# Performance work log

Measured on AMD Instinct MI355X. Metric: run time of the kernel, lower is better.

The kernel has to match this reference:

```python
import jax, jax.numpy as jnp
import numpy as np

BATCH, SEQ, STATE, OBS, INP = 4096, 512, 16, 8, 4


def setup_inputs() -> dict:
    key = jax.random.key(0)
    ks = jax.random.split(key, 5)
    # scale A to spectral radius ~0.3 so the 512-step recursion is stable
    A = jax.random.normal(ks[0], (STATE, STATE), jnp.float32) * (0.3 / np.sqrt(STATE))
    B = jax.random.normal(ks[1], (STATE, INP), jnp.float32) * 0.1
    C = jax.random.normal(ks[2], (OBS, STATE), jnp.float32) * (1.0 / np.sqrt(STATE))
    Q = jnp.eye(STATE, dtype=jnp.float32)   # module default when Q is None
    R = jnp.eye(OBS, dtype=jnp.float32)     # module default when R is None
    x0 = jnp.zeros((STATE,), jnp.float32)   # module default initial_state_mean
    obs = jax.random.normal(ks[3], (BATCH, SEQ, OBS), jnp.float32)
    u = jax.random.normal(ks[4], (BATCH, SEQ, INP), jnp.float32)
    return {"obs": obs, "u": u, "A": A, "B": B, "C": C, "Q": Q, "R": R, "x0": x0}


def reference(obs, u, A, B, C, Q, R, x0):
    Bsz = obs.shape[0]
    S = A.shape[0]
    eyeS = jnp.eye(S, dtype=obs.dtype)
    x_init = jnp.broadcast_to(x0, (Bsz, S))                 # (B,S), P0 = I per module init
    P_init = jnp.broadcast_to(eyeS, (Bsz, S, S))

    def step(carry, inp):
        x, P = carry                                        # x:(B,S)  P:(B,S,S)
        u_k, z_k = inp                                      # (B,I), (B,O)
        # stage 1: prediction
        x_prior = x @ A.T + u_k @ B.T                       # (B,S)
        P_prior = A @ P @ A.T + Q                           # (B,S,S)
        # stage 2: measurement update
        Smat = C @ P_prior @ C.T + R                        # (B,O,O) innovation covariance
        K = P_prior @ C.T @ jnp.linalg.inv(Smat)            # (B,S,O)
        innov = z_k - x_prior @ C.T                         # (B,O)
        x_post = x_prior + jnp.einsum('bso,bo->bs', K, innov)
        P_post = (eyeS - K @ C) @ P_prior                   # (B,S,S)
        return (x_post, P_post), x_post

    inp_seq = (jnp.swapaxes(u, 0, 1), jnp.swapaxes(obs, 0, 1))  # time-major for scan
    _, xs = jax.lax.scan(step, (x_init, P_init), inp_seq)       # xs: (T,B,S)
    return jnp.swapaxes(xs, 0, 1)                               # (B,T,S) == states_est[:,1:,:]
```

## Files before the change

### kernel.cpp

```cpp
#include <hip/hip_runtime.h>
#include <hip/hip_bf16.h>

#define SEQ   512
#define BATCH 4096
#define NS    16
#define NO    8
#define NI    4
#define NK    12
#define CH    16
#define CL    (SEQ/CH)
#define CW    8

__device__ __align__(16) float g_gains[NK * 448];
__device__ int   g_isf32_data;
__device__ __align__(16) float g_x0[NS];

typedef __attribute__((ext_vector_type(4))) _Float16 h4;
typedef __attribute__((ext_vector_type(4))) float    f4;

static __device__ __forceinline__ float bf2f_us(unsigned short v) {
    unsigned int u = ((unsigned int)v) << 16;
    return __uint_as_float(u);
}

static __device__ __forceinline__ float4 ld4(const float* p) { return *(const float4*)p; }
static __device__ __forceinline__ void st4(float* p, float4 v) { *(float4*)p = v; }
static __device__ __forceinline__ void fma4(float4& a, float s, float4 b) {
    a.x += s*b.x; a.y += s*b.y; a.z += s*b.z; a.w += s*b.w;
}
static __device__ __forceinline__ void fnma4(float4& a, float s, float4 b) {
    a.x -= s*b.x; a.y -= s*b.y; a.z -= s*b.z; a.w -= s*b.w;
}

__global__ __launch_bounds__(64) void riccati_kernel(
        const void* __restrict__ Ap, const void* __restrict__ Bp,
        const void* __restrict__ Cp, const void* __restrict__ Qp,
        const void* __restrict__ Rp, const void* __restrict__ x0p,
        const void* __restrict__ obsp) {
    __shared__ __align__(16) float A[NS*NS], AT[NS*NS], Q[NS*NS];
    __shared__ __align__(16) float P[NS*NS], AP[NS*NS], Pp[NS*NS];
    __shared__ __align__(16) float Cm[NO*NS], CT[NS*NO], Bm[NS*NI], R[NO*NO];
    __shared__ __align__(16) float CA[NO*NS], CB[NO*NI];
    __shared__ __align__(16) float CP[NO*NS], PCt[NS*NO], K[NS*NO];
    __shared__ __align__(16) float G[NO*2*NO];
    __shared__ int sflag_p, sflag_d;

    const int t  = threadIdx.x;
    const int i  = t >> 2;
    const int jq = t & 3;
    const int j0 = jq * 4;

    if (t == 0) { sflag_p = 0; sflag_d = 0; }
    __syncthreads();
    {
        const unsigned short* ah = (const unsigned short*)Ap;
        for (int s = 0; s < 4; ++s) {
            float v = fabsf(bf2f_us(ah[t + 64*s]));
            if (!(v < 16.0f)) sflag_p = 1;
        }
        const unsigned short* oh = (const unsigned short*)obsp;
        for (int s = 0; s < 32; ++s) {
            float w = fabsf(bf2f_us(oh[t + 64*s]));
            if (!(w < 16.0f)) sflag_d = 1;
        }
    }
    __syncthreads();
    const bool f32p = (sflag_p != 0);
    if (t == 0) g_isf32_data = (sflag_d != 0) ? 1 : 0;

    auto ld = [&](const void* p, int idx) -> float {
        return f32p ? ((const float*)p)[idx]
                    : bf2f_us(((const unsigned short*)p)[idx]);
    };

    for (int q = t; q < NS*NS; q += 64) {
        A[q] = ld(Ap, q);
        Q[q] = ld(Qp, q);
        P[q] = ((q >> 4) == (q & 15)) ? 1.0f : 0.0f;
    }
    Bm[t] = ld(Bp, t);
    for (int q = t; q < NO*NS; q += 64) Cm[q] = ld(Cp, q);
    R[t] = ld(Rp, t);
    if (t < NS) g_x0[t] = ld(x0p, t);
    __syncthreads();

    for (int q = t; q < NS*NS; q += 64) AT[(q & 15)*NS + (q >> 4)] = A[q];
    for (int q = t; q < NO*NS; q += 64) CT[(q & 15)*NO + (q >> 4)] = Cm[q];
    if (t < 32) {
        const int io = t >> 2;
        float4 acc = make_float4(0.f, 0.f, 0.f, 0.f);
        for (int l = 0; l < NS; ++l) fma4(acc, Cm[io*NS + l], ld4(&A[l*NS + j0]));
        st4(&CA[io*NS + j0], acc);
    } else if (t < 40) {
        const int io = t - 32;
        float4 acc = make_float4(0.f, 0.f, 0.f, 0.f);
        for (int l = 0; l < NS; ++l) fma4(acc, Cm[io*NS + l], ld4(&Bm[l*NI]));
        st4(&CB[io*NI], acc);
    }
    __syncthreads();

    for (int k = 0; k < NK; ++k) {
        {
            float4 acc = make_float4(0.f, 0.f, 0.f, 0.f);
            for (int l = 0; l < NS; ++l) fma4(acc, A[i*NS + l], ld4(&P[l*NS + j0]));
            st4(&AP[i*NS + j0], acc);
        }
        __syncthreads();
        {
            float4 acc = ld4(&Q[i*NS + j0]);
            for (int l = 0; l < NS; ++l) fma4(acc, AP[i*NS + l], ld4(&AT[l*NS + j0]));
            st4(&Pp[i*NS + j0], acc);
        }
        __syncthreads();
        if (t < 32) {
            const int io = t >> 2;
            float4 acc = make_float4(0.f, 0.f, 0.f, 0.f);
            for (int l = 0; l < NS; ++l) fma4(acc, Cm[io*NS + l], ld4(&Pp[l*NS + j0]));
            st4(&CP[io*NS + j0], acc);
        } else {
            const int t2 = t - 32;
            const int i2 = t2 >> 1, jb = (t2 & 1) * 4;
            float4 acc = make_float4(0.f, 0.f, 0.f, 0.f);
            for (int l = 0; l < NS; ++l) fma4(acc, Pp[i2*NS + l], ld4(&CT[l*NO + jb]));
            st4(&PCt[i2*NO + jb], acc);
        }
        __syncthreads();
        if (t < 32) {
            const int io = t >> 2;
            if (jq < 2) {
                float4 acc = ld4(&R[io*NO + j0]);
                for (int l = 0; l < NS; ++l) fma4(acc, CP[io*NS + l], ld4(&CT[l*NO + j0]));
                st4(&G[io*2*NO + j0], acc);
            } else {
                float4 v = make_float4((j0 + 0 - NO) == io ? 1.f : 0.f,
                                       (j0 + 1 - NO) == io ? 1.f : 0.f,
                                       (j0 + 2 - NO) == io ? 1.f : 0.f,
                                       (j0 + 3 - NO) == io ? 1.f : 0.f);
                st4(&G[io*2*NO + j0], v);
            }
        }
        __syncthreads();
        for (int p = 0; p < NO; ++p) {
            float piv = 1.f, gip = 0.f;
            float4 gp4 = make_float4(0.f, 0.f, 0.f, 0.f);
            float4 g4  = make_float4(0.f, 0.f, 0.f, 0.f);
            if (t < 32) {
                const int io = t >> 2;
                piv = G[p*2*NO + p];
                gip = G[io*2*NO + p];
                gp4 = ld4(&G[p*2*NO + j0]);
                g4  = ld4(&G[io*2*NO + j0]);
            }
            __syncthreads();
            if (t < 32) {
                const int io = t >> 2;
                const float inv = 1.0f / piv;
                float4 r4 = make_float4(gp4.x*inv, gp4.y*inv, gp4.z*inv, gp4.w*inv);
                float4 w;
                if (io == p) w = r4;
                else w = make_float4(g4.x - gip*r4.x, g4.y - gip*r4.y,
                                     g4.z - gip*r4.z, g4.w - gip*r4.w);
                st4(&G[io*2*NO + j0], w);
            }
            __syncthreads();
        }
        if (t < 32) {
            const int i2 = t >> 1, jb = (t & 1) * 4;
            float4 acc = make_float4(0.f, 0.f, 0.f, 0.f);
            for (int l = 0; l < NO; ++l) fma4(acc, PCt[i2*NO + l], ld4(&G[l*2*NO + NO + jb]));
            st4(&K[i2*NO + jb], acc);
        }
        __syncthreads();
        float* outp = g_gains + k * 448;
        {
            float4 m4 = ld4(&A[i*NS + j0]);
            float4 pn = ld4(&Pp[i*NS + j0]);
            for (int l = 0; l < NO; ++l) {
                const float kk = K[i*NO + l];
                fnma4(m4, kk, ld4(&CA[l*NS + j0]));
                fnma4(pn, kk, ld4(&CP[l*NS + j0]));
            }
            st4(outp + i*NS + j0, m4);
            st4(&P[i*NS + j0], pn);
        }
        if (jq == 0) {
            float4 n4 = ld4(&Bm[i*NI]);
            for (int l = 0; l < NO; ++l) fnma4(n4, K[i*NO + l], ld4(&CB[l*NI]));
            st4(outp + 256 + i*NI, n4);
        } else if (jq < 3) {
            const int jb = (jq - 1) * 4;
            st4(outp + 320 + i*NO + jb, ld4(&K[i*NO + jb]));
        }
        __syncthreads();
    }
}


static __device__ __forceinline__ void split4(float a, float b, float c, float d,
                                              h4& hi, h4& lo) {
    _Float16 ha = (_Float16)a, hb = (_Float16)b, hc = (_Float16)c, hd = (_Float16)d;
    hi = (h4){ha, hb, hc, hd};
    lo = (h4){(_Float16)(a - (float)ha), (_Float16)(b - (float)hb),
              (_Float16)(c - (float)hc), (_Float16)(d - (float)hd)};
}

struct AF { h4 mh, ml, ah, al; };

static __device__ __forceinline__ void load_af(const float* __restrict__ gb,
                                               int row, int g, AF& F) {
    float4 m = ld4(gb + row*NS + g*4);
    split4(m.x, m.y, m.z, m.w, F.mh, F.ml);
    float4 a;
    if      (g == 0) a = ld4(gb + 256 + row*NI);
    else if (g == 1) a = ld4(gb + 320 + row*NO);
    else if (g == 2) a = ld4(gb + 320 + row*NO + 4);
    else             a = make_float4(0.f, 0.f, 0.f, 0.f);
    split4(a.x, a.y, a.z, a.w, F.ah, F.al);
}

static __device__ __forceinline__ f4 stept(const AF& F, f4 X,
                                           float i0, float i1, float i2, float i3) {
    h4 xh, xl, bh, bl;
    split4(X.x, X.y, X.z, X.w, xh, xl);
    split4(i0, i1, i2, i3, bh, bl);
    f4 acc = {0.f, 0.f, 0.f, 0.f};
    acc = __builtin_amdgcn_mfma_f32_16x16x16f16(F.mh, xh, acc, 0, 0, 0);
    acc = __builtin_amdgcn_mfma_f32_16x16x16f16(F.mh, xl, acc, 0, 0, 0);
    acc = __builtin_amdgcn_mfma_f32_16x16x16f16(F.ml, xh, acc, 0, 0, 0);
    acc = __builtin_amdgcn_mfma_f32_16x16x16f16(F.ah, bh, acc, 0, 0, 0);
    acc = __builtin_amdgcn_mfma_f32_16x16x16f16(F.ah, bl, acc, 0, 0, 0);
    acc = __builtin_amdgcn_mfma_f32_16x16x16f16(F.al, bh, acc, 0, 0, 0);
    return acc;
}

static __device__ __forceinline__ float4 up2(uint2 v) {
    return make_float4(bf2f_us(v.x & 0xffffu), bf2f_us(v.x >> 16),
                       bf2f_us(v.y & 0xffffu), bf2f_us(v.y >> 16));
}

template<bool F32, bool C0>
static __device__ __forceinline__ void run_tile(
        const void* __restrict__ obsv, const void* __restrict__ uv,
        float* __restrict__ out, int c, int eb) {
    const int lane = threadIdx.x & 63;
    const int n = lane & 15, g = lane >> 4;
    const int cL = c * CL, k0 = C0 ? 0 : (cL - CW), kend = cL + CL;

    AF F;
    load_af(C0 ? g_gains : (g_gains + (NK-1)*448), n, g, F);

    f4 X;
    if (C0) {
        float4 xi = ld4(&g_x0[g*4]);
        X = (f4){xi.x, xi.y, xi.z, xi.w};
    } else {
        X = (f4){0.f, 0.f, 0.f, 0.f};
    }

    const int e = eb + n;
    float* o = out + (size_t)e * SEQ * NS + g*4;

    const int st = (g == 0) ? NI : NO;

    if (F32) {
        const float* p = (g == 0)
            ? ((const float*)uv   + ((size_t)e*SEQ + k0)*NI)
            : ((const float*)obsv + ((size_t)e*SEQ + k0)*NO + ((g >= 2) ? 4 : 0));
        float4 cur = ld4(p), nxt = ld4(p + st);
        for (int k = k0; k < kend; ++k) {
            float4 v = cur; cur = nxt;
            if (k + 2 < kend) nxt = ld4(p + 2*st);
            p += st;
            X = stept(F, X, v.x, v.y, v.z, v.w);
            if (C0 && (k + 1) < NK) load_af(g_gains + (size_t)(k+1)*448, n, g, F);
            if (k >= cL) *(f4*)(o + (size_t)k * NS) = X;
        }
    } else {
        const unsigned short* p = (g == 0)
            ? ((const unsigned short*)uv   + ((size_t)e*SEQ + k0)*NI)
            : ((const unsigned short*)obsv + ((size_t)e*SEQ + k0)*NO + ((g >= 2) ? 4 : 0));
        uint2 cur = *(const uint2*)p, nxt = *(const uint2*)(p + st);
        for (int k = k0; k < kend; ++k) {
            float4 v = up2(cur); cur = nxt;
            if (k + 2 < kend) nxt = *(const uint2*)(p + 2*st);
            p += st;
            X = stept(F, X, v.x, v.y, v.z, v.w);
            if (C0 && (k + 1) < NK) load_af(g_gains + (size_t)(k+1)*448, n, g, F);
            if (k >= cL) *(f4*)(o + (size_t)k * NS) = X;
        }
    }
}

__global__ __launch_bounds__(256) void filter_kernel(
        const void* __restrict__ obs, const void* __restrict__ u,
        float* __restrict__ out) {
    const int W  = blockIdx.x * 4 + (threadIdx.x >> 6);
    const int c  = W >> 8;
    const int eb = (W & 255) * 16;
    if (g_isf32_data) {
        if (c == 0) run_tile<true,  true >(obs, u, out, c, eb);
        else        run_tile<true,  false>(obs, u, out, c, eb);
    } else {
        if (c == 0) run_tile<false, true >(obs, u, out, c, eb);
        else        run_tile<false, false>(obs, u, out, c, eb);
    }
}

extern "C" void kernel_launch(void* const* d_in, const int* in_sizes, int n_in,
                              void* d_out, int out_size, void* d_ws, size_t ws_size,
                              hipStream_t stream) {
    const void* obs = d_in[0];
    const void* u   = d_in[1];
    const void* A   = d_in[2];
    const void* B   = d_in[3];
    const void* C   = d_in[4];
    const void* Q   = d_in[5];
    const void* R   = d_in[6];
    const void* x0  = d_in[7];
    float* out = (float*)d_out;

    riccati_kernel<<<1, 64, 0, stream>>>(A, B, C, Q, R, x0, obs);
    filter_kernel<<<dim3(CH * 256 / 4), dim3(256), 0, stream>>>(obs, u, out);
}
```

Baseline: 338.0 us.

## Stage obs/u inputs through shared memory with coalesced block-wide loads

The filter kernel now loads 8-timestep stages of u and obs for 64 batch elements cooperatively across the block, using coalesced global loads. These are written into a swizzled shared-memory buffer, and each lane reads its own timestep from there instead of doing strided per-lane global loads. Output stores are paired so two consecutive timesteps are written together. This adds two __syncthreads per stage and ties the four waves of a block together, which can stall the latency-bound recurrence.

```diff
diff --git a/kernel.cpp b/kernel.cpp
--- a/kernel.cpp
+++ b/kernel.cpp
@@ -10,6 +10,7 @@
 #define CH    16
 #define CL    (SEQ/CH)
 #define CW    8
+#define TSTG  8
 
 __device__ __align__(16) float g_gains[NK * 448];
 __device__ int   g_isf32_data;
@@ -238,13 +239,17 @@
                        bf2f_us(v.y & 0xffffu), bf2f_us(v.y >> 16));
 }
 
+static __device__ __forceinline__ int swz(int t, int r) { return (t*192 + r) ^ t; }
+
 template<bool F32, bool C0>
 static __device__ __forceinline__ void run_tile(
         const void* __restrict__ obsv, const void* __restrict__ uv,
-        float* __restrict__ out, int c, int eb) {
-    const int lane = threadIdx.x & 63;
+        float* __restrict__ out, int c, int EB0, float4* sb4) {
+    const int tid  = threadIdx.x;
+    const int lane = tid & 63, w = tid >> 6;
     const int n = lane & 15, g = lane >> 4;
     const int cL = c * CL, k0 = C0 ? 0 : (cL - CW), kend = cL + CL;
+    const int NSTG = (kend - k0) >> 3;
 
     AF F;
     load_af(C0 ? g_gains : (g_gains + (NK-1)*448), n, g, F);
@@ -256,53 +261,96 @@
     } else {
         X = (f4){0.f, 0.f, 0.f, 0.f};
     }
-
-    const int e = eb + n;
+    f4 Xe = X;
+
+    const int ew = w*16 + n;
+    const int e  = EB0 + ew;
     float* o = out + (size_t)e * SEQ * NS + g*4;
-
-    const int st = (g == 0) ? NI : NO;
-
-    if (F32) {
-        const float* p = (g == 0)
-            ? ((const float*)uv   + ((size_t)e*SEQ + k0)*NI)
-            : ((const float*)obsv + ((size_t)e*SEQ + k0)*NO + ((g >= 2) ? 4 : 0));
-        float4 cur = ld4(p), nxt = ld4(p + st);
-        for (int k = k0; k < kend; ++k) {
-            float4 v = cur; cur = nxt;
-            if (k + 2 < kend) nxt = ld4(p + 2*st);
-            p += st;
+    const int rb = ew*3 + ((g >= 2) ? 2 : g);
+
+    float4 ru0, ru1, rz0, rz1, rz2, rz3;
+    uint2  bu0, bu1;  uint4 bz0, bz1;
+
+    auto ldstage = [&](int ks) {
+        if (F32) {
+            const float* uf = (const float*)uv;
+            const float* zf = (const float*)obsv;
+            { int j = tid;       ru0 = ld4(uf + ((size_t)(EB0+(j>>3))*SEQ + ks + (j&7))*NI); }
+            { int j = tid + 256; ru1 = ld4(uf + ((size_t)(EB0+(j>>3))*SEQ + ks + (j&7))*NI); }
+            { int j = tid;       rz0 = ld4(zf + ((size_t)(EB0+(j>>4))*SEQ + ks + ((j&15)>>1))*NO + (j&1)*4); }
+            { int j = tid + 256; rz1 = ld4(zf + ((size_t)(EB0+(j>>4))*SEQ + ks + ((j&15)>>1))*NO + (j&1)*4); }
+            { int j = tid + 512; rz2 = ld4(zf + ((size_t)(EB0+(j>>4))*SEQ + ks + ((j&15)>>1))*NO + (j&1)*4); }
+            { int j = tid + 768; rz3 = ld4(zf + ((size_t)(EB0+(j>>4))*SEQ + ks + ((j&15)>>1))*NO + (j&1)*4); }
+        } else {
+            const unsigned short* ub = (const unsigned short*)uv;
+            const unsigned short* zb = (const unsigned short*)obsv;
+            { int j = tid;       bu0 = *(const uint2*)(ub + ((size_t)(EB0+(j>>3))*SEQ + ks + (j&7))*NI); }
+            { int j = tid + 256; bu1 = *(const uint2*)(ub + ((size_t)(EB0+(j>>3))*SEQ + ks + (j&7))*NI); }
+            { int j = tid;       bz0 = *(const uint4*)(zb + ((size_t)(EB0+(j>>3))*SEQ + ks + (j&7))*NO); }
+            { int j = tid + 256; bz1 = *(const uint4*)(zb + ((size_t)(EB0+(j>>3))*SEQ + ks + (j&7))*NO); }
+        }
+    };
+    auto wrstage = [&]() {
+        if (F32) {
+            { int j = tid;       sb4[swz(j&7, (j>>3)*3)] = ru0; }
+            { int j = tid + 256; sb4[swz(j&7, (j>>3)*3)] = ru1; }
+            { int j = tid;       sb4[swz((j&15)>>1, (j>>4)*3 + 1 + (j&1))] = rz0; }
+            { int j = tid + 256; sb4[swz((j&15)>>1, (j>>4)*3 + 1 + (j&1))] = rz1; }
+            { int j = tid + 512; sb4[swz((j&15)>>1, (j>>4)*3 + 1 + (j&1))] = rz2; }
+            { int j = tid + 768; sb4[swz((j&15)>>1, (j>>4)*3 + 1 + (j&1))] = rz3; }
+        } else {
+            { int j = tid;       sb4[swz(j&7, (j>>3)*3)] = up2(bu0); }
+            { int j = tid + 256; sb4[swz(j&7, (j>>3)*3)] = up2(bu1); }
+            { int j = tid;
+              sb4[swz(j&7, (j>>3)*3 + 1)] = up2(make_uint2(bz0.x, bz0.y));
+              sb4[swz(j&7, (j>>3)*3 + 2)] = up2(make_uint2(bz0.z, bz0.w)); }
+            { int j = tid + 256;
+              sb4[swz(j&7, (j>>3)*3 + 1)] = up2(make_uint2(bz1.x, bz1.y));
+              sb4[swz(j&7, (j>>3)*3 + 2)] = up2(make_uint2(bz1.z, bz1.w)); }
+        }
+    };
+
+    ldstage(k0);
+    wrstage();
+    __syncthreads();
+
+    for (int s = 0; s < NSTG; ++s) {
+        const int ks = k0 + s * TSTG;
+        const bool more = (s + 1 < NSTG);
+        if (more) ldstage(ks + TSTG);
+#pragma unroll
+        for (int t = 0; t < TSTG; ++t) {
+            const int k = ks + t;
+            float4 v = sb4[swz(t, rb)];
             X = stept(F, X, v.x, v.y, v.z, v.w);
             if (C0 && (k + 1) < NK) load_af(g_gains + (size_t)(k+1)*448, n, g, F);
-            if (k >= cL) *(f4*)(o + (size_t)k * NS) = X;
-        }
-    } else {
-        const unsigned short* p = (g == 0)
-            ? ((const unsigned short*)uv   + ((size_t)e*SEQ + k0)*NI)
-            : ((const unsigned short*)obsv + ((size_t)e*SEQ + k0)*NO + ((g >= 2) ? 4 : 0));
-        uint2 cur = *(const uint2*)p, nxt = *(const uint2*)(p + st);
-        for (int k = k0; k < kend; ++k) {
-            float4 v = up2(cur); cur = nxt;
-            if (k + 2 < kend) nxt = *(const uint2*)(p + 2*st);
-            p += st;
-            X = stept(F, X, v.x, v.y, v.z, v.w);
-            if (C0 && (k + 1) < NK) load_af(g_gains + (size_t)(k+1)*448, n, g, F);
-            if (k >= cL) *(f4*)(o + (size_t)k * NS) = X;
-        }
+            if (k >= cL) {
+                if ((k & 1) == 0) {
+                    Xe = X;
+                } else {
+                    *(f4*)(o + (size_t)(k-1) * NS) = Xe;
+                    *(f4*)(o + (size_t)k     * NS) = X;
+                }
+            }
+        }
+        __syncthreads();
+        if (more) wrstage();
+        __syncthreads();
     }
 }
 
 __global__ __launch_bounds__(256) void filter_kernel(
         const void* __restrict__ obs, const void* __restrict__ u,
         float* __restrict__ out) {
-    const int W  = blockIdx.x * 4 + (threadIdx.x >> 6);
-    const int c  = W >> 8;
-    const int eb = (W & 255) * 16;
+    __shared__ __align__(16) float4 sb4[TSTG * 64 * 3];
+    const int c   = blockIdx.x >> 6;
+    const int EB0 = (blockIdx.x & 63) * 64;
     if (g_isf32_data) {
-        if (c == 0) run_tile<true,  true >(obs, u, out, c, eb);
-        else        run_tile<true,  false>(obs, u, out, c, eb);
+        if (c == 0) run_tile<true,  true >(obs, u, out, c, EB0, sb4);
+        else        run_tile<true,  false>(obs, u, out, c, EB0, sb4);
     } else {
-        if (c == 0) run_tile<false, true >(obs, u, out, c, eb);
-        else        run_tile<false, false>(obs, u, out, c, eb);
+        if (c == 0) run_tile<false, true >(obs, u, out, c, EB0, sb4);
+        else        run_tile<false, false>(obs, u, out, c, EB0, sb4);
     }
 }
 
@@ -320,5 +368,5 @@
     float* out = (float*)d_out;
 
     riccati_kernel<<<1, 64, 0, stream>>>(A, B, C, Q, R, x0, obs);
-    filter_kernel<<<dim3(CH * 256 / 4), dim3(256), 0, stream>>>(obs, u, out);
-}
+    filter_kernel<<<dim3(CH * 64), dim3(256), 0, stream>>>(obs, u, out);
+}
```

Result: faster. 292.4 us (-13.5%).
